# Kernel optimization log

Measured on AMD Instinct MI355X. Metric: run time of the kernel, lower is better.

The kernel has to match this reference:

```python
import jax, jax.numpy as jnp
import numpy as np

P = 4   # patch_size
S = 2   # patch_stride


def setup_inputs() -> dict:
    key = jax.random.key(0)
    ks = jax.random.split(key, 7)
    img    = jax.random.uniform(ks[0], (8, 1, 1024, 1024), dtype=jnp.float32)
    w_conv = jax.random.normal(ks[1], (2, 1, 2, 2), dtype=jnp.float32) * 0.5  # Conv2d(1,2,k=2,s=2)
    b_conv = jax.random.normal(ks[2], (2,), dtype=jnp.float32) * 0.1
    W_b    = jax.random.normal(ks[3], (2, 2), dtype=jnp.float32) * 0.5        # Linear(2,2)
    b_b    = jax.random.normal(ks[4], (2,), dtype=jnp.float32) * 0.1
    W_d    = jax.random.normal(ks[5], (2, 1, 2, 2), dtype=jnp.float32) * 0.5  # ConvTranspose2d(2,1,k=2,s=2)
    b_d    = jax.random.normal(ks[6], (1,), dtype=jnp.float32) * 0.1
    return dict(img=img, w_conv=w_conv, b_conv=b_conv, W_b=W_b, b_b=b_b, W_d=W_d, b_d=b_d)


def reference(img, w_conv, b_conv, W_b, b_b, W_d, b_d):
    B, _, H, Wd_ = img.shape
    nj = (H - P) // S + 1
    nk = (Wd_ - P) // S + 1

    # gather indices for patch extraction / overlap-add
    rows = (jnp.arange(nj) * S)[:, None] + jnp.arange(P)[None, :]  # (nj, P)
    cols = (jnp.arange(nk) * S)[:, None] + jnp.arange(P)[None, :]  # (nk, P)
    r = rows[:, None, :, None]  # (nj, 1, P, 1)
    c = cols[None, :, None, :]  # (1, nk, 1, P)

    # extract all overlapping patches: (B, nj, nk, P, P)
    patches = img[:, 0][:, r, c]
    N = B * nj * nk
    p = patches.reshape(N, P, P)

    # Conv2d(1->2, kernel 2, stride 2) + ReLU; non-overlapping 2x2 blocks
    blocks = p.reshape(N, 2, 2, 2, 2)                 # (N, j2, ph, k2, pw)
    conv = jnp.einsum('njpkq,cpq->ncjk', blocks, w_conv[:, 0]) + b_conv[None, :, None, None]
    conv = jax.nn.relu(conv)                          # (N, 2, 2, 2)

    # MaxPool2d(2,2) with indices (row-major within 2x2 window)
    flat = conv.reshape(N, 2, 4)
    idx = jnp.argmax(flat, axis=-1)                   # (N, 2) int
    vals = jnp.max(flat, axis=-1)                     # (N, 2)

    # bottleneck: Linear(2,2) + ReLU
    z = jax.nn.relu(vals @ W_b.T + b_b)               # (N, 2)

    # MaxUnpool2d -> (N, 2, 2, 2)
    unp = (z[..., None] * jax.nn.one_hot(idx, 4, dtype=z.dtype)).reshape(N, 2, 2, 2)

    # ConvTranspose2d(2->1, kernel 2, stride 2) + Sigmoid: out[2i+p, 2j+q]
    dec = jnp.einsum('ncij,cpq->nipjq', unp, W_d[:, 0]).reshape(N, P, P) + b_d[0]
    dec = jax.nn.sigmoid(dec).reshape(B, nj, nk, P, P)

    # overlap-add fold + count normalization
    out = jnp.zeros((B, H, Wd_), dtype=img.dtype).at[:, r, c].add(dec)
    count = jnp.zeros((H, Wd_), dtype=img.dtype).at[r, c].add(1.0)
    return (out / count)[:, None]  # (B, 1, H, W)
```

## Files before the change

kernel.cpp:

```cpp
#include <hip/hip_runtime.h>

#define IMG_H 1024
#define IMG_W 1024
#define TILES 16
#define NPJ 17
#define NPATCH (NPJ * NPJ)
#define PSTRH 20

typedef __attribute__((ext_vector_type(2))) __fp16 h2;

static __device__ __forceinline__ float h2_as_f(h2 v) {
    union { h2 h; float f; } u; u.h = v; return u.f;
}
static __device__ __forceinline__ h2 f_as_h2(float f) {
    union { float f; h2 h; } u; u.f = f; return u.h;
}

__global__ __launch_bounds__(256) void ae_fused(
    const float* __restrict__ img,
    const float* __restrict__ w_conv,
    const float* __restrict__ b_conv,
    const float* __restrict__ W_b,
    const float* __restrict__ b_b,
    const float* __restrict__ W_d,
    const float* __restrict__ b_d,
    float* __restrict__ out)
{
    __shared__ __align__(16) __fp16 dec[NPATCH * PSTRH];

    const int t  = threadIdx.x;
    const int n0 = blockIdx.x * TILES;
    const int m0 = blockIdx.y * TILES;
    const int b  = blockIdx.z;

    const float LOG2E = 1.4426950408889634f;
    float wc[2][4], nwd[2][4], wb[2][2];
    #pragma unroll
    for (int c = 0; c < 2; ++c) {
        #pragma unroll
        for (int q = 0; q < 4; ++q) {
            wc[c][q]  = w_conv[c * 4 + q];
            nwd[c][q] = -W_d[c * 4 + q] * LOG2E;
        }
    }
    wb[0][0] = W_b[0]; wb[0][1] = W_b[1];
    wb[1][0] = W_b[2]; wb[1][1] = W_b[3];
    const float bc0 = b_conv[0], bc1 = b_conv[1];
    const float bb0 = b_b[0],   bb1 = b_b[1];
    const float nbd = -b_d[0] * LOG2E;
    const float scf = 1.0f / (1.0f + exp2f(nbd));
    const h2 ch = { (__fp16)scf, (__fp16)scf };
    const h2 zh = { (__fp16)0.0f, (__fp16)0.0f };

    const float* imgb = img + (size_t)b * IMG_H * IMG_W;

    #pragma unroll
    for (int it = 0; it < 2; ++it) {
        const int lp = t + it * 256;
        if (lp < NPATCH) {
            const int lpj = lp / NPJ;
            const int lpk = lp - lpj * NPJ;
            const int j = m0 - 1 + lpj;
            const int k = n0 - 1 + lpk;
            __fp16* d = &dec[lp * PSTRH];
            if (j >= 0 && j <= 510 && k >= 0 && k <= 510) {
                const float* base = imgb + (size_t)(2 * j) * IMG_W + 2 * k;
                float v0[4], v1[4];
                #pragma unroll
                for (int jj = 0; jj < 2; ++jj) {
                    #pragma unroll
                    for (int kk = 0; kk < 2; ++kk) {
                        const float2 ra = *(const float2*)(base + (size_t)(2 * jj) * IMG_W + 2 * kk);
                        const float2 rb = *(const float2*)(base + (size_t)(2 * jj + 1) * IMG_W + 2 * kk);
                        const float s0 = ra.x * wc[0][0] + ra.y * wc[0][1] + rb.x * wc[0][2] + rb.y * wc[0][3] + bc0;
                        const float s1 = ra.x * wc[1][0] + ra.y * wc[1][1] + rb.x * wc[1][2] + rb.y * wc[1][3] + bc1;
                        v0[jj * 2 + kk] = fmaxf(s0, 0.0f);
                        v1[jj * 2 + kk] = fmaxf(s1, 0.0f);
                    }
                }
                int i0 = 0, i1 = 0;
                float mx0 = v0[0], mx1 = v1[0];
                #pragma unroll
                for (int q = 1; q < 4; ++q) {
                    if (v0[q] > mx0) { mx0 = v0[q]; i0 = q; }
                    if (v1[q] > mx1) { mx1 = v1[q]; i1 = q; }
                }
                const float z0 = fmaxf(mx0 * wb[0][0] + mx1 * wb[0][1] + bb0, 0.0f);
                const float z1 = fmaxf(mx0 * wb[1][0] + mx1 * wb[1][1] + bb1, 0.0f);

                const float ag1 = (i1 == i0) ? z1 : 0.0f;
                const float bg0 = (i0 == i1) ? z0 : 0.0f;
                float av[4], bv[4];
                #pragma unroll
                for (int q = 0; q < 4; ++q) {
                    av[q] = 1.0f / (1.0f + exp2f(z0 * nwd[0][q] + ag1 * nwd[1][q] + nbd));
                    bv[q] = 1.0f / (1.0f + exp2f(bg0 * nwd[0][q] + z1 * nwd[1][q] + nbd));
                }
                const h2 a01 = __builtin_amdgcn_cvt_pkrtz(av[0], av[1]);
                const h2 a23 = __builtin_amdgcn_cvt_pkrtz(av[2], av[3]);
                const h2 b01 = __builtin_amdgcn_cvt_pkrtz(bv[0], bv[1]);
                const h2 b23 = __builtin_amdgcn_cvt_pkrtz(bv[2], bv[3]);
                #pragma unroll
                for (int qd = 0; qd < 4; ++qd) {
                    const h2 q01 = (qd == i1) ? b01 : ((qd == i0) ? a01 : ch);
                    const h2 q23 = (qd == i1) ? b23 : ((qd == i0) ? a23 : ch);
                    float2 w; w.x = h2_as_f(q01); w.y = h2_as_f(q23);
                    *(float2*)(d + 4 * qd) = w;
                }
            } else {
                float2 zw; zw.x = h2_as_f(zh); zw.y = h2_as_f(zh);
                #pragma unroll
                for (int qd = 0; qd < 4; ++qd) *(float2*)(d + 4 * qd) = zw;
            }
        }
    }
    __syncthreads();

    const int ty = t >> 4, tx = t & 15;
    const int m = m0 + ty, n = n0 + tx;
    h2 s01 = zh, s23 = zh;
    #pragma unroll
    for (int a = 0; a < 2; ++a) {
        #pragma unroll
        for (int e = 0; e < 2; ++e) {
            const int lp = (ty + a) * NPJ + (tx + e);
            const int qd = (1 - a) * 2 + (1 - e);
            const float2 w = *(const float2*)(dec + lp * PSTRH + 4 * qd);
            s01 += f_as_h2(w.x);
            s23 += f_as_h2(w.y);
        }
    }
    const float rcnt = 1.0f / (float)(((m >= 1) + (m <= 510)) * ((n >= 1) + (n <= 510)));
    float* outb = out + (size_t)b * IMG_H * IMG_W;
    *(float2*)(outb + (size_t)(2 * m) * IMG_W + 2 * n) =
        make_float2((float)s01.x * rcnt, (float)s01.y * rcnt);
    *(float2*)(outb + (size_t)(2 * m + 1) * IMG_W + 2 * n) =
        make_float2((float)s23.x * rcnt, (float)s23.y * rcnt);
}

extern "C" void kernel_launch(void* const* d_in, const int* in_sizes, int n_in,
                              void* d_out, int out_size, void* d_ws, size_t ws_size,
                              hipStream_t stream) {
    const float* img    = (const float*)d_in[0];
    const float* w_conv = (const float*)d_in[1];
    const float* b_conv = (const float*)d_in[2];
    const float* W_b    = (const float*)d_in[3];
    const float* b_b    = (const float*)d_in[4];
    const float* W_d    = (const float*)d_in[5];
    const float* b_d    = (const float*)d_in[6];
    float* out = (float*)d_out;

    dim3 block(256, 1, 1);
    dim3 grid(512 / TILES, 512 / TILES, 8);
    ae_fused<<<grid, block, 0, stream>>>(img, w_conv, b_conv, W_b, b_b, W_d, b_d, out);
}
```

Before: 112.1 us.

## Use 15x15 output tiles so one thread computes exactly one patch

Output tiles shrink from 16x16 to 15x15, so the 16x16 patch halo maps one-to-one onto the 256 threads. This removes the second patch-iteration pass (289 patches over 256 threads) and the division-based indexing. The grid grows to 35x35 blocks with bounds checks, and the dec writes become a constant fill followed by indexed overwrites instead of selects. In exchange, halo recompute rises, about 12% of threads sit idle in the output phase, and occupancy is hinted with launch_bounds(256,4).

```diff
diff --git a/kernel.cpp b/kernel.cpp
--- a/kernel.cpp
+++ b/kernel.cpp
@@ -2,10 +2,11 @@
 
 #define IMG_H 1024
 #define IMG_W 1024
-#define TILES 16
-#define NPJ 17
+#define TILES 15
+#define NPJ 16
 #define NPATCH (NPJ * NPJ)
 #define PSTRH 20
+#define NBLK 35
 
 typedef __attribute__((ext_vector_type(2))) __fp16 h2;
 
@@ -16,7 +17,7 @@
     union { float f; h2 h; } u; u.f = f; return u.h;
 }
 
-__global__ __launch_bounds__(256) void ae_fused(
+__global__ __launch_bounds__(256, 4) void ae_fused(
     const float* __restrict__ img,
     const float* __restrict__ w_conv,
     const float* __restrict__ b_conv,
@@ -29,6 +30,7 @@
     __shared__ __align__(16) __fp16 dec[NPATCH * PSTRH];
 
     const int t  = threadIdx.x;
+    const int ty = t >> 4, tx = t & 15;
     const int n0 = blockIdx.x * TILES;
     const int m0 = blockIdx.y * TILES;
     const int b  = blockIdx.z;
@@ -54,88 +56,83 @@
 
     const float* imgb = img + (size_t)b * IMG_H * IMG_W;
 
-    #pragma unroll
-    for (int it = 0; it < 2; ++it) {
-        const int lp = t + it * 256;
-        if (lp < NPATCH) {
-            const int lpj = lp / NPJ;
-            const int lpk = lp - lpj * NPJ;
-            const int j = m0 - 1 + lpj;
-            const int k = n0 - 1 + lpk;
-            __fp16* d = &dec[lp * PSTRH];
-            if (j >= 0 && j <= 510 && k >= 0 && k <= 510) {
-                const float* base = imgb + (size_t)(2 * j) * IMG_W + 2 * k;
-                float v0[4], v1[4];
+    {
+        const int j = m0 - 1 + ty;
+        const int k = n0 - 1 + tx;
+        __fp16* d = &dec[t * PSTRH];
+        if (j >= 0 && j <= 510 && k >= 0 && k <= 510) {
+            const int off = (j << 11) + (k << 1);
+            float v0[4], v1[4];
+            #pragma unroll
+            for (int jj = 0; jj < 2; ++jj) {
                 #pragma unroll
-                for (int jj = 0; jj < 2; ++jj) {
-                    #pragma unroll
-                    for (int kk = 0; kk < 2; ++kk) {
-                        const float2 ra = *(const float2*)(base + (size_t)(2 * jj) * IMG_W + 2 * kk);
-                        const float2 rb = *(const float2*)(base + (size_t)(2 * jj + 1) * IMG_W + 2 * kk);
-                        const float s0 = ra.x * wc[0][0] + ra.y * wc[0][1] + rb.x * wc[0][2] + rb.y * wc[0][3] + bc0;
-                        const float s1 = ra.x * wc[1][0] + ra.y * wc[1][1] + rb.x * wc[1][2] + rb.y * wc[1][3] + bc1;
-                        v0[jj * 2 + kk] = fmaxf(s0, 0.0f);
-                        v1[jj * 2 + kk] = fmaxf(s1, 0.0f);
-                    }
+                for (int kk = 0; kk < 2; ++kk) {
+                    const float2 ra = *(const float2*)(imgb + off + (jj << 11) + (kk << 1));
+                    const float2 rb = *(const float2*)(imgb + off + (jj << 11) + (kk << 1) + IMG_W);
+                    const float s0 = ra.x * wc[0][0] + ra.y * wc[0][1] + rb.x * wc[0][2] + rb.y * wc[0][3] + bc0;
+                    const float s1 = ra.x * wc[1][0] + ra.y * wc[1][1] + rb.x * wc[1][2] + rb.y * wc[1][3] + bc1;
+                    v0[jj * 2 + kk] = fmaxf(s0, 0.0f);
+                    v1[jj * 2 + kk] = fmaxf(s1, 0.0f);
                 }
-                int i0 = 0, i1 = 0;
-                float mx0 = v0[0], mx1 = v1[0];
-                #pragma unroll
-                for (int q = 1; q < 4; ++q) {
-                    if (v0[q] > mx0) { mx0 = v0[q]; i0 = q; }
-                    if (v1[q] > mx1) { mx1 = v1[q]; i1 = q; }
-                }
-                const float z0 = fmaxf(mx0 * wb[0][0] + mx1 * wb[0][1] + bb0, 0.0f);
-                const float z1 = fmaxf(mx0 * wb[1][0] + mx1 * wb[1][1] + bb1, 0.0f);
+            }
+            int i0 = 0, i1 = 0;
+            float mx0 = v0[0], mx1 = v1[0];
+            #pragma unroll
+            for (int q = 1; q < 4; ++q) {
+                if (v0[q] > mx0) { mx0 = v0[q]; i0 = q; }
+                if (v1[q] > mx1) { mx1 = v1[q]; i1 = q; }
+            }
+            const float z0 = fmaxf(mx0 * wb[0][0] + mx1 * wb[0][1] + bb0, 0.0f);
+            const float z1 = fmaxf(mx0 * wb[1][0] + mx1 * wb[1][1] + bb1, 0.0f);
 
-                const float ag1 = (i1 == i0) ? z1 : 0.0f;
-                const float bg0 = (i0 == i1) ? z0 : 0.0f;
-                float av[4], bv[4];
-                #pragma unroll
-                for (int q = 0; q < 4; ++q) {
-                    av[q] = 1.0f / (1.0f + exp2f(z0 * nwd[0][q] + ag1 * nwd[1][q] + nbd));
-                    bv[q] = 1.0f / (1.0f + exp2f(bg0 * nwd[0][q] + z1 * nwd[1][q] + nbd));
-                }
-                const h2 a01 = __builtin_amdgcn_cvt_pkrtz(av[0], av[1]);
-                const h2 a23 = __builtin_amdgcn_cvt_pkrtz(av[2], av[3]);
-                const h2 b01 = __builtin_amdgcn_cvt_pkrtz(bv[0], bv[1]);
-                const h2 b23 = __builtin_amdgcn_cvt_pkrtz(bv[2], bv[3]);
-                #pragma unroll
-                for (int qd = 0; qd < 4; ++qd) {
-                    const h2 q01 = (qd == i1) ? b01 : ((qd == i0) ? a01 : ch);
-                    const h2 q23 = (qd == i1) ? b23 : ((qd == i0) ? a23 : ch);
-                    float2 w; w.x = h2_as_f(q01); w.y = h2_as_f(q23);
-                    *(float2*)(d + 4 * qd) = w;
-                }
-            } else {
-                float2 zw; zw.x = h2_as_f(zh); zw.y = h2_as_f(zh);
-                #pragma unroll
-                for (int qd = 0; qd < 4; ++qd) *(float2*)(d + 4 * qd) = zw;
+            const float ag1 = (i1 == i0) ? z1 : 0.0f;
+            const float bg0 = (i0 == i1) ? z0 : 0.0f;
+            float av[4], bv[4];
+            #pragma unroll
+            for (int q = 0; q < 4; ++q) {
+                av[q] = 1.0f / (1.0f + exp2f(z0 * nwd[0][q] + ag1 * nwd[1][q] + nbd));
+                bv[q] = 1.0f / (1.0f + exp2f(bg0 * nwd[0][q] + z1 * nwd[1][q] + nbd));
             }
+            float2 cw; cw.x = h2_as_f(ch); cw.y = h2_as_f(ch);
+            #pragma unroll
+            for (int qd = 0; qd < 4; ++qd) *(float2*)(d + 4 * qd) = cw;
+            float2 aw; aw.x = h2_as_f(__builtin_amdgcn_cvt_pkrtz(av[0], av[1]));
+                       aw.y = h2_as_f(__builtin_amdgcn_cvt_pkrtz(av[2], av[3]));
+            *(float2*)(d + 4 * i0) = aw;
+            float2 bw; bw.x = h2_as_f(__builtin_amdgcn_cvt_pkrtz(bv[0], bv[1]));
+                       bw.y = h2_as_f(__builtin_amdgcn_cvt_pkrtz(bv[2], bv[3]));
+            *(float2*)(d + 4 * i1) = bw;
+        } else {
+            float2 zw; zw.x = h2_as_f(zh); zw.y = h2_as_f(zh);
+            #pragma unroll
+            for (int qd = 0; qd < 4; ++qd) *(float2*)(d + 4 * qd) = zw;
         }
     }
     __syncthreads();
 
-    const int ty = t >> 4, tx = t & 15;
-    const int m = m0 + ty, n = n0 + tx;
-    h2 s01 = zh, s23 = zh;
-    #pragma unroll
-    for (int a = 0; a < 2; ++a) {
-        #pragma unroll
-        for (int e = 0; e < 2; ++e) {
-            const int lp = (ty + a) * NPJ + (tx + e);
-            const int qd = (1 - a) * 2 + (1 - e);
-            const float2 w = *(const float2*)(dec + lp * PSTRH + 4 * qd);
-            s01 += f_as_h2(w.x);
-            s23 += f_as_h2(w.y);
+    if (ty < TILES && tx < TILES) {
+        const int m = m0 + ty, n = n0 + tx;
+        if (m < 512 && n < 512) {
+            h2 s01 = zh, s23 = zh;
+            #pragma unroll
+            for (int a = 0; a < 2; ++a) {
+                #pragma unroll
+                for (int e = 0; e < 2; ++e) {
+                    const int lp = ((ty + a) << 4) + (tx + e);
+                    const int qd = (1 - a) * 2 + (1 - e);
+                    const float2 w = *(const float2*)(dec + lp * PSTRH + 4 * qd);
+                    s01 += f_as_h2(w.x);
+                    s23 += f_as_h2(w.y);
+                }
+            }
+            const float rcnt = 1.0f / (float)(((m >= 1) + (m <= 510)) * ((n >= 1) + (n <= 510)));
+            float* outb = out + (size_t)b * IMG_H * IMG_W;
+            *(float2*)(outb + (size_t)(2 * m) * IMG_W + 2 * n) =
+                make_float2((float)s01.x * rcnt, (float)s01.y * rcnt);
+            *(float2*)(outb + (size_t)(2 * m + 1) * IMG_W + 2 * n) =
+                make_float2((float)s23.x * rcnt, (float)s23.y * rcnt);
         }
     }
-    const float rcnt = 1.0f / (float)(((m >= 1) + (m <= 510)) * ((n >= 1) + (n <= 510)));
-    float* outb = out + (size_t)b * IMG_H * IMG_W;
-    *(float2*)(outb + (size_t)(2 * m) * IMG_W + 2 * n) =
-        make_float2((float)s01.x * rcnt, (float)s01.y * rcnt);
-    *(float2*)(outb + (size_t)(2 * m + 1) * IMG_W + 2 * n) =
-        make_float2((float)s23.x * rcnt, (float)s23.y * rcnt);
 }
 
 extern "C" void kernel_launch(void* const* d_in, const int* in_sizes, int n_in,
@@ -151,6 +148,6 @@
     float* out = (float*)d_out;
 
     dim3 block(256, 1, 1);
-    dim3 grid(512 / TILES, 512 / TILES, 8);
+    dim3 grid(NBLK, NBLK, 8);
     ae_fused<<<grid, block, 0, stream>>>(img, w_conv, b_conv, W_b, b_b, W_d, b_d, out);
 }
```

Result: faster. 108.1 us (-3.6%).
